# Optimization experiments

Measured on AMD Instinct MI355X. Metric: run time of the kernel, lower is better.

The kernel has to match this reference:

```python
import jax, jax.numpy as jnp
import numpy as np

NUM_HEADS = 16

def _apply_rope(t, cos, sin):
    # t: [B, nh, S, hd]; cos/sin: [S, hd//2]
    t1 = t[..., 0::2]
    t2 = t[..., 1::2]
    c = cos[None, None, :, :]
    s = sin[None, None, :, :]
    r1 = t1 * c - t2 * s
    r2 = t1 * s + t2 * c
    # interleave back to [..., hd]
    out = jnp.stack([r1, r2], axis=-1)
    return out.reshape(t.shape)

def setup_inputs() -> dict:
    key = jax.random.key(0)
    ks = jax.random.split(key, 6)
    B, S, H = 1, 4096, 1024
    hd = H // NUM_HEADS
    x = jax.random.normal(ks[0], (B, S, H), dtype=jnp.float32)
    # RoPE angle matrix: theta[pos, i] = pos / 10000^(2i/hd), shape [context, hd//2]
    pos = jnp.arange(S, dtype=jnp.float32)[:, None]
    inv_freq = 1.0 / (10000.0 ** (jnp.arange(0, hd, 2, dtype=jnp.float32) / hd))
    rotation = pos * inv_freq[None, :]
    sc = 1.0 / np.sqrt(H)
    W_qkv = jax.random.normal(ks[1], (H, 3 * H), dtype=jnp.float32) * sc
    b_qkv = jax.random.normal(ks[2], (3 * H,), dtype=jnp.float32) * 0.01
    W_out = jax.random.normal(ks[3], (H, H), dtype=jnp.float32) * sc
    b_out = jax.random.normal(ks[4], (H,), dtype=jnp.float32) * 0.01
    return {"x": x, "rotation": rotation, "W_qkv": W_qkv, "b_qkv": b_qkv,
            "W_out": W_out, "b_out": b_out, "window_size": 33}

def reference(x, rotation, W_qkv, b_qkv, W_out, b_out, window_size):
    B, S, H = x.shape
    nh = NUM_HEADS
    hd = H // nh
    W = window_size
    pad = W // 2
    qkv = x @ W_qkv + b_qkv                               # [B, S, 3H]
    qkv = qkv.reshape(B, S, nh, 3 * hd).transpose(0, 2, 1, 3)  # [B, nh, S, 3hd]
    q, k, v = jnp.split(qkv, 3, axis=-1)                  # each [B, nh, S, hd]
    cos = jnp.cos(rotation[:S])
    sin = jnp.sin(rotation[:S])
    q = _apply_rope(q, cos, sin)
    k = _apply_rope(k, cos, sin)
    # zero-pad along sequence, then gather sliding windows
    k_pad = jnp.pad(k, ((0, 0), (0, 0), (pad, pad), (0, 0)))
    v_pad = jnp.pad(v, ((0, 0), (0, 0), (pad, pad), (0, 0)))
    idx = jnp.arange(S)[:, None] + jnp.arange(W)[None, :]  # [S, W]
    k_win = k_pad[:, :, idx, :]                            # [B, nh, S, W, hd]
    v_win = v_pad[:, :, idx, :]
    scores = jnp.einsum('bnsh,bnswh->bnsw', q, k_win) / np.sqrt(hd)
    attn = jax.nn.softmax(scores, axis=-1)
    ctx = jnp.einsum('bnsw,bnswh->bnsh', attn, v_win)      # [B, nh, S, hd]
    ctx = ctx.transpose(0, 2, 1, 3).reshape(B, S, H)
    return ctx @ W_out + b_out
```

## Files before the change

kernel.cpp:

```cpp
#include <hip/hip_runtime.h>
#include <hip/hip_bf16.h>

#define S_LEN 4096
#define NH 16
#define HD 64
#define WIN 33
#define PAD 16
#define QT 64
#define KROWS 96
#define KPITCH_U 36

#define BM 128
#define BN 128
#define BK 64

typedef short short8 __attribute__((ext_vector_type(8)));
typedef float f32x4 __attribute__((ext_vector_type(4)));

__device__ __forceinline__ float bl(unsigned u){ return __uint_as_float(u << 16); }
__device__ __forceinline__ float bh(unsigned u){ return __uint_as_float(u & 0xffff0000u); }
__device__ __forceinline__ unsigned f2bfu(float f){
  unsigned u = __float_as_uint(f);
  return (u + 0x7fffu + ((u >> 16) & 1u)) >> 16;
}
__device__ __forceinline__ unsigned pack2(float a, float b){ return f2bfu(a) | (f2bfu(b) << 16); }

__device__ __forceinline__ void gload_lds16(const void* g, void* l){
  __builtin_amdgcn_global_load_lds(
      (const __attribute__((address_space(1))) void*)g,
      (__attribute__((address_space(3))) void*)l, 16, 0, 0);
}


__global__ __launch_bounds__(256) void rope_table(const float* __restrict__ rot,
                                                  float* __restrict__ cost,
                                                  float* __restrict__ sint, int n){
  int t = blockIdx.x * 256 + threadIdx.x;
  if (t < n) {
    float v = rot[t], sv, cv;
    sincosf(v, &sv, &cv);
    cost[t] = cv; sint[t] = sv;
  }
}

__global__ __launch_bounds__(256) void f32_to_bf16_vec(const float* __restrict__ in,
                                                       __hip_bfloat16* __restrict__ out){
  int t = blockIdx.x * 256 + threadIdx.x;
  const float4* p = (const float4*)in + (size_t)t * 2;
  float4 a = p[0], b = p[1];
  uint4 o;
  o.x = pack2(a.x, a.y); o.y = pack2(a.z, a.w);
  o.z = pack2(b.x, b.y); o.w = pack2(b.z, b.w);
  ((uint4*)out)[t] = o;
}

__global__ __launch_bounds__(256) void transpose_f32_to_bf16(const float* __restrict__ in,
                                                             __hip_bfloat16* __restrict__ out,
                                                             int R, int C){
  __shared__ float tile[32][33];
  int c0 = blockIdx.x * 32, r0 = blockIdx.y * 32;
  int tx = threadIdx.x, ty = threadIdx.y;
  #pragma unroll
  for (int i = 0; i < 4; ++i) {
    int r = ty + i * 8;
    tile[r][tx] = in[(size_t)(r0 + r) * C + c0 + tx];
  }
  __syncthreads();
  #pragma unroll
  for (int i = 0; i < 4; ++i) {
    int cc = ty + i * 8;
    ((unsigned short*)out)[(size_t)(c0 + cc) * R + r0 + tx] = (unsigned short)f2bfu(tile[tx][cc]);
  }
}


__global__ __launch_bounds__(256) void gemm_qkv_rope(
    const __hip_bfloat16* __restrict__ A,
    const __hip_bfloat16* __restrict__ Bt,
    const float* __restrict__ bias,
    const float* __restrict__ cost,
    const float* __restrict__ sint,
    unsigned short* __restrict__ Cout,
    int M, int N, int K)
{
  __shared__ unsigned int lA[BM * BK / 2];
  __shared__ unsigned int lB[BN * BK / 2];
  const int tid = threadIdx.x;
  const int wave = tid >> 6, lane = tid & 63;
  const int m0 = blockIdx.y * BM, n0 = blockIdx.x * BN;
  const int wm = (wave >> 1) * 64, wn = (wave & 1) * 64;
  const int l16 = lane >> 4, l15 = lane & 15;

  f32x4 acc[4][4];
  #pragma unroll
  for (int i = 0; i < 4; ++i)
    #pragma unroll
    for (int j = 0; j < 4; ++j) acc[i][j] = (f32x4){0.f, 0.f, 0.f, 0.f};

  const int nkt = K / BK;
  for (int kt = 0; kt < nkt; ++kt) {
    __syncthreads();
    #pragma unroll
    for (int it = 0; it < 4; ++it) {
      const int c = it * 256 + wave * 64 + lane;
      const int r = c >> 3, s8 = c & 7;
      const int ss = s8 ^ (r & 7);
      gload_lds16(A  + (size_t)(m0 + r) * K + kt * BK + ss * 8,
                  (char*)lA + (it * 256 + wave * 64) * 16);
      gload_lds16(Bt + (size_t)(n0 + r) * K + kt * BK + ss * 8,
                  (char*)lB + (it * 256 + wave * 64) * 16);
    }
    __syncthreads();
    #pragma unroll
    for (int ks = 0; ks < 2; ++ks) {
      short8 af[4], bfr[4];
      #pragma unroll
      for (int mi = 0; mi < 4; ++mi) {
        const int r = wm + mi * 16 + l15;
        const int slot = (ks * 4 + l16) ^ (r & 7);
        uint4 u = *(const uint4*)((const char*)lA + r * 128 + slot * 16);
        af[mi] = __builtin_bit_cast(short8, u);
      }
      #pragma unroll
      for (int ni = 0; ni < 4; ++ni) {
        const int r = wn + ni * 16 + l15;
        const int slot = (ks * 4 + l16) ^ (r & 7);
        uint4 u = *(const uint4*)((const char*)lB + r * 128 + slot * 16);
        bfr[ni] = __builtin_bit_cast(short8, u);
      }
      #pragma unroll
      for (int mi = 0; mi < 4; ++mi)
        #pragma unroll
        for (int ni = 0; ni < 4; ++ni)
          acc[mi][ni] = __builtin_amdgcn_mfma_f32_16x16x32_bf16(af[mi], bfr[ni], acc[mi][ni], 0, 0, 0);
    }
  }

  #pragma unroll
  for (int ni = 0; ni < 4; ++ni) {
    const int cn = n0 + wn + ni * 16 + l15;
    const int rseg = cn % 192;
    const float bv = bias[cn];
    if (rseg < 128) {
      const int i = (rseg & 63) >> 1;
      const float sgn = (cn & 1) ? 1.f : -1.f;
      #pragma unroll
      for (int mi = 0; mi < 4; ++mi) {
        #pragma unroll
        for (int j = 0; j < 4; ++j) {
          const int rm = m0 + wm + mi * 16 + l16 * 4 + j;
          const float v = acc[mi][ni][j] + bv;
          const float p = __shfl_xor(v, 1);
          const float cc = cost[rm * 32 + i], ss = sint[rm * 32 + i];
          const float res = v * cc + p * (sgn * ss);
          Cout[(size_t)rm * N + cn] = (unsigned short)f2bfu(res);
        }
      }
    } else {
      #pragma unroll
      for (int mi = 0; mi < 4; ++mi) {
        #pragma unroll
        for (int j = 0; j < 4; ++j) {
          const int rm = m0 + wm + mi * 16 + l16 * 4 + j;
          Cout[(size_t)rm * N + cn] = (unsigned short)f2bfu(acc[mi][ni][j] + bv);
        }
      }
    }
  }
}


__global__ __launch_bounds__(256) void gemm_small(
    const __hip_bfloat16* __restrict__ A,
    const __hip_bfloat16* __restrict__ Bt,
    const float* __restrict__ bias,
    float* __restrict__ Cout,
    int M, int N, int K)
{
  __shared__ unsigned int lA[64 * 64 / 2];
  __shared__ unsigned int lB[64 * 64 / 2];
  const int tid = threadIdx.x;
  const int wave = tid >> 6, lane = tid & 63;
  const int m0 = blockIdx.y * 64, n0 = blockIdx.x * 64;
  const int wm = (wave >> 1) * 32, wn = (wave & 1) * 32;
  const int l16 = lane >> 4, l15 = lane & 15;

  f32x4 acc[2][2];
  #pragma unroll
  for (int i = 0; i < 2; ++i)
    #pragma unroll
    for (int j = 0; j < 2; ++j) acc[i][j] = (f32x4){0.f, 0.f, 0.f, 0.f};

  const int nkt = K / 64;
  for (int kt = 0; kt < nkt; ++kt) {
    __syncthreads();
    #pragma unroll
    for (int it = 0; it < 2; ++it) {
      const int c = it * 256 + wave * 64 + lane;
      const int r = c >> 3, s8 = c & 7;
      const int ss = s8 ^ (r & 7);
      gload_lds16(A  + (size_t)(m0 + r) * K + kt * 64 + ss * 8,
                  (char*)lA + (it * 256 + wave * 64) * 16);
      gload_lds16(Bt + (size_t)(n0 + r) * K + kt * 64 + ss * 8,
                  (char*)lB + (it * 256 + wave * 64) * 16);
    }
    __syncthreads();
    #pragma unroll
    for (int ks = 0; ks < 2; ++ks) {
      short8 af[2], bfr[2];
      #pragma unroll
      for (int mi = 0; mi < 2; ++mi) {
        const int r = wm + mi * 16 + l15;
        const int slot = (ks * 4 + l16) ^ (r & 7);
        uint4 u = *(const uint4*)((const char*)lA + r * 128 + slot * 16);
        af[mi] = __builtin_bit_cast(short8, u);
      }
      #pragma unroll
      for (int ni = 0; ni < 2; ++ni) {
        const int r = wn + ni * 16 + l15;
        const int slot = (ks * 4 + l16) ^ (r & 7);
        uint4 u = *(const uint4*)((const char*)lB + r * 128 + slot * 16);
        bfr[ni] = __builtin_bit_cast(short8, u);
      }
      #pragma unroll
      for (int mi = 0; mi < 2; ++mi)
        #pragma unroll
        for (int ni = 0; ni < 2; ++ni)
          acc[mi][ni] = __builtin_amdgcn_mfma_f32_16x16x32_bf16(af[mi], bfr[ni], acc[mi][ni], 0, 0, 0);
    }
  }

  #pragma unroll
  for (int ni = 0; ni < 2; ++ni) {
    const int cn = n0 + wn + ni * 16 + l15;
    const float bv = bias[cn];
    #pragma unroll
    for (int mi = 0; mi < 2; ++mi) {
      #pragma unroll
      for (int j = 0; j < 4; ++j) {
        const int rm = m0 + wm + mi * 16 + l16 * 4 + j;
        Cout[(size_t)rm * N + cn] = acc[mi][ni][j] + bv;
      }
    }
  }
}


__global__ __launch_bounds__(256) void attn_kernel(const __hip_bfloat16* __restrict__ qkv,
                                                   __hip_bfloat16* __restrict__ ctx){
  __shared__ unsigned int kbuf[KROWS * KPITCH_U];
  __shared__ unsigned int vbuf[KROWS * KPITCH_U];
  const int tid = threadIdx.x;
  const int h   = blockIdx.x & 15;
  const int qs0 = (blockIdx.x >> 4) * QT;

  #pragma unroll
  for (int it = 0; it < 3; ++it) {
    int c = tid + it * 256;
    int r = c >> 3, s8 = c & 7;
    int srow = qs0 - PAD + r;
    uint4 kv = make_uint4(0, 0, 0, 0), vv = make_uint4(0, 0, 0, 0);
    if ((unsigned)srow < (unsigned)S_LEN) {
      kv = ((const uint4*)(qkv + (size_t)srow * 3072 + h * 192 + 64))[s8];
      vv = ((const uint4*)(qkv + (size_t)srow * 3072 + h * 192 + 128))[s8];
    }
    *(uint4*)(kbuf + r * KPITCH_U + s8 * 4) = kv;
    *(uint4*)(vbuf + r * KPITCH_U + s8 * 4) = vv;
  }

  const int ql = tid >> 2, t4 = tid & 3;
  const uint4* qp = (const uint4*)(qkv + (size_t)(qs0 + ql) * 3072 + h * 192);
  float qf[64];
  #pragma unroll
  for (int c = 0; c < 8; ++c) {
    uint4 v = qp[c];
    qf[c*8+0] = bl(v.x); qf[c*8+1] = bh(v.x);
    qf[c*8+2] = bl(v.y); qf[c*8+3] = bh(v.y);
    qf[c*8+4] = bl(v.z); qf[c*8+5] = bh(v.z);
    qf[c*8+6] = bl(v.w); qf[c*8+7] = bh(v.w);
  }
  __syncthreads();

  float sc[9];
  #pragma unroll
  for (int j = 0; j < 9; ++j) sc[j] = 0.f;
  float mx = -1e30f;
  #pragma unroll
  for (int j = 0; j < 9; ++j) {
    int w = t4 + 4 * j;
    if (w < WIN) {
      int rw = ql + w;
      const uint4* kp = (const uint4*)(kbuf + rw * KPITCH_U);
      float d = 0.f;
      #pragma unroll
      for (int c = 0; c < 8; ++c) {
        uint4 kv = kp[c];
        d += qf[c*8+0]*bl(kv.x) + qf[c*8+1]*bh(kv.x)
           + qf[c*8+2]*bl(kv.y) + qf[c*8+3]*bh(kv.y)
           + qf[c*8+4]*bl(kv.z) + qf[c*8+5]*bh(kv.z)
           + qf[c*8+6]*bl(kv.w) + qf[c*8+7]*bh(kv.w);
      }
      sc[j] = d * 0.125f;
      mx = fmaxf(mx, sc[j]);
    }
  }
  mx = fmaxf(mx, __shfl_xor(mx, 1));
  mx = fmaxf(mx, __shfl_xor(mx, 2));
  float sum = 0.f;
  #pragma unroll
  for (int j = 0; j < 9; ++j) {
    int w = t4 + 4 * j;
    if (w < WIN) { sc[j] = __expf(sc[j] - mx); sum += sc[j]; }
  }
  sum += __shfl_xor(sum, 1);
  sum += __shfl_xor(sum, 2);
  const float inv = 1.0f / sum;
  #pragma unroll
  for (int j = 0; j < 9; ++j) sc[j] *= inv;

  float accd[16];
  #pragma unroll
  for (int i = 0; i < 16; ++i) accd[i] = 0.f;
  #pragma unroll
  for (int w = 0; w < WIN; ++w) {
    float wgt = __shfl(sc[w >> 2], ((tid & 63) & ~3) | (w & 3), 64);
    int rw = ql + w;
    const uint4* vp = (const uint4*)(vbuf + rw * KPITCH_U + t4 * 8);
    uint4 a = vp[0], b = vp[1];
    float vf[16];
    vf[0]=bl(a.x); vf[1]=bh(a.x); vf[2]=bl(a.y); vf[3]=bh(a.y);
    vf[4]=bl(a.z); vf[5]=bh(a.z); vf[6]=bl(a.w); vf[7]=bh(a.w);
    vf[8]=bl(b.x); vf[9]=bh(b.x); vf[10]=bl(b.y); vf[11]=bh(b.y);
    vf[12]=bl(b.z); vf[13]=bh(b.z); vf[14]=bl(b.w); vf[15]=bh(b.w);
    #pragma unroll
    for (int i = 0; i < 16; ++i) accd[i] += wgt * vf[i];
  }

  unsigned short* op = (unsigned short*)ctx + (size_t)(qs0 + ql) * 1024 + h * 64 + t4 * 16;
  uint4 o1, o2;
  o1.x = pack2(accd[0], accd[1]);  o1.y = pack2(accd[2], accd[3]);
  o1.z = pack2(accd[4], accd[5]);  o1.w = pack2(accd[6], accd[7]);
  o2.x = pack2(accd[8], accd[9]);  o2.y = pack2(accd[10], accd[11]);
  o2.z = pack2(accd[12], accd[13]); o2.w = pack2(accd[14], accd[15]);
  *(uint4*)op = o1;
  *((uint4*)op + 1) = o2;
}


extern "C" void kernel_launch(void* const* d_in, const int* in_sizes, int n_in,
                              void* d_out, int out_size, void* d_ws, size_t ws_size,
                              hipStream_t stream)
{
  const float* x     = (const float*)d_in[0];
  const float* rot   = (const float*)d_in[1];
  const float* W_qkv = (const float*)d_in[2];
  const float* b_qkv = (const float*)d_in[3];
  const float* W_out = (const float*)d_in[4];
  const float* b_out = (const float*)d_in[5];
  float* out = (float*)d_out;

  char* ws = (char*)d_ws;
  __hip_bfloat16* xb   = (__hip_bfloat16*)(ws + 0);
  __hip_bfloat16* Wt1  = (__hip_bfloat16*)(ws + 8388608);
  __hip_bfloat16* Wt2  = (__hip_bfloat16*)(ws + 14680064);
  __hip_bfloat16* qkvb = (__hip_bfloat16*)(ws + 16777216);
  __hip_bfloat16* ctx  = (__hip_bfloat16*)(ws + 41943040);
  float* cost          = (float*)(ws + 50331648);
  float* sint          = (float*)(ws + 50855936);

  rope_table<<<512, 256, 0, stream>>>(rot, cost, sint, S_LEN * 32);
  f32_to_bf16_vec<<<2048, 256, 0, stream>>>(x, xb);
  transpose_f32_to_bf16<<<dim3(96, 32), dim3(32, 8), 0, stream>>>(W_qkv, Wt1, 1024, 3072);
  transpose_f32_to_bf16<<<dim3(32, 32), dim3(32, 8), 0, stream>>>(W_out, Wt2, 1024, 1024);
  gemm_qkv_rope<<<dim3(3072 / BN, 4096 / BM), 256, 0, stream>>>(xb, Wt1, b_qkv, cost, sint,
                                                                (unsigned short*)qkvb, 4096, 3072, 1024);
  attn_kernel<<<64 * 16, 256, 0, stream>>>(qkvb, ctx);
  gemm_small<<<dim3(1024 / 64, 4096 / 64), 256, 0, stream>>>(ctx, Wt2, b_out, out, 4096, 1024, 1024);
}
```

Measured before the change: 105.6 us.

## Merge prep kernels, double-buffer GEMMs, swizzle blocks, retile output GEMM

Merges the four preprocessing kernels (RoPE table, x conversion, two weight transposes) into one launch, and packs cos/sin into one float2 table computed with the fast __sincosf intrinsic. Both GEMMs now double-buffer LDS so the next K tile loads while the current one is multiplied. They also remap block indices for L2 locality and raise wave priority around the MFMA loops. The output GEMM moves from 64x64 to 128x64 tiles. The cost is more LDS per block, which may lower occupancy, and __sincosf gives less accurate sin/cos.

```diff
diff --git a/kernel.cpp b/kernel.cpp
--- a/kernel.cpp
+++ b/kernel.cpp
@@ -32,44 +32,44 @@
 }
 
 
-__global__ __launch_bounds__(256) void rope_table(const float* __restrict__ rot,
-                                                  float* __restrict__ cost,
-                                                  float* __restrict__ sint, int n){
-  int t = blockIdx.x * 256 + threadIdx.x;
-  if (t < n) {
+__global__ __launch_bounds__(256) void prep_all(
+    const float* __restrict__ rot, float2* __restrict__ csq,
+    const float* __restrict__ x, __hip_bfloat16* __restrict__ xb,
+    const float* __restrict__ Wq, __hip_bfloat16* __restrict__ Wt1,
+    const float* __restrict__ Wo, __hip_bfloat16* __restrict__ Wt2)
+{
+  __shared__ float tile[32][33];
+  const int b = blockIdx.x, tid = threadIdx.x;
+  if (b < 512) {
+    int t = b * 256 + tid;
     float v = rot[t], sv, cv;
-    sincosf(v, &sv, &cv);
-    cost[t] = cv; sint[t] = sv;
-  }
-}
-
-__global__ __launch_bounds__(256) void f32_to_bf16_vec(const float* __restrict__ in,
-                                                       __hip_bfloat16* __restrict__ out){
-  int t = blockIdx.x * 256 + threadIdx.x;
-  const float4* p = (const float4*)in + (size_t)t * 2;
-  float4 a = p[0], b = p[1];
-  uint4 o;
-  o.x = pack2(a.x, a.y); o.y = pack2(a.z, a.w);
-  o.z = pack2(b.x, b.y); o.w = pack2(b.z, b.w);
-  ((uint4*)out)[t] = o;
-}
-
-__global__ __launch_bounds__(256) void transpose_f32_to_bf16(const float* __restrict__ in,
-                                                             __hip_bfloat16* __restrict__ out,
-                                                             int R, int C){
-  __shared__ float tile[32][33];
-  int c0 = blockIdx.x * 32, r0 = blockIdx.y * 32;
-  int tx = threadIdx.x, ty = threadIdx.y;
-  #pragma unroll
-  for (int i = 0; i < 4; ++i) {
-    int r = ty + i * 8;
-    tile[r][tx] = in[(size_t)(r0 + r) * C + c0 + tx];
-  }
-  __syncthreads();
-  #pragma unroll
-  for (int i = 0; i < 4; ++i) {
-    int cc = ty + i * 8;
-    ((unsigned short*)out)[(size_t)(c0 + cc) * R + r0 + tx] = (unsigned short)f2bfu(tile[tx][cc]);
+    __sincosf(v, &sv, &cv);
+    csq[t] = make_float2(cv, sv);
+  } else if (b < 2560) {
+    int t = (b - 512) * 256 + tid;
+    const float4* p = (const float4*)x + (size_t)t * 2;
+    float4 a = p[0], c = p[1];
+    uint4 o;
+    o.x = pack2(a.x, a.y); o.y = pack2(a.z, a.w);
+    o.z = pack2(c.x, c.y); o.w = pack2(c.z, c.w);
+    ((uint4*)xb)[t] = o;
+  } else {
+    const float* in; unsigned short* out; int R, C, bx, by;
+    if (b < 5632) { int bb = b - 2560; in = Wq; out = (unsigned short*)Wt1; R = 1024; C = 3072; bx = bb % 96; by = bb / 96; }
+    else          { int bb = b - 5632; in = Wo; out = (unsigned short*)Wt2; R = 1024; C = 1024; bx = bb % 32; by = bb / 32; }
+    int c0 = bx * 32, r0 = by * 32;
+    int tx = tid & 31, ty = tid >> 5;
+    #pragma unroll
+    for (int i = 0; i < 4; ++i) {
+      int r = ty + i * 8;
+      tile[r][tx] = in[(size_t)(r0 + r) * C + c0 + tx];
+    }
+    __syncthreads();
+    #pragma unroll
+    for (int i = 0; i < 4; ++i) {
+      int cc = ty + i * 8;
+      out[(size_t)(c0 + cc) * R + r0 + tx] = (unsigned short)f2bfu(tile[tx][cc]);
+    }
   }
 }
 
@@ -78,16 +78,17 @@
     const __hip_bfloat16* __restrict__ A,
     const __hip_bfloat16* __restrict__ Bt,
     const float* __restrict__ bias,
-    const float* __restrict__ cost,
-    const float* __restrict__ sint,
+    const float2* __restrict__ csq,
     unsigned short* __restrict__ Cout,
     int M, int N, int K)
 {
-  __shared__ unsigned int lA[BM * BK / 2];
-  __shared__ unsigned int lB[BN * BK / 2];
+  __shared__ unsigned int lA[2][BM * BK / 2];
+  __shared__ unsigned int lB[2][BN * BK / 2];
   const int tid = threadIdx.x;
   const int wave = tid >> 6, lane = tid & 63;
-  const int m0 = blockIdx.y * BM, n0 = blockIdx.x * BN;
+  const int flat = blockIdx.y * 24 + blockIdx.x;
+  const int swz = (flat & 7) * 96 + (flat >> 3);
+  const int m0 = (swz / 24) * BM, n0 = (swz % 24) * BN;
   const int wm = (wave >> 1) * 64, wn = (wave & 1) * 64;
   const int l16 = lane >> 4, l15 = lane & 15;
 
@@ -97,20 +98,25 @@
     #pragma unroll
     for (int j = 0; j < 4; ++j) acc[i][j] = (f32x4){0.f, 0.f, 0.f, 0.f};
 
-  const int nkt = K / BK;
-  for (int kt = 0; kt < nkt; ++kt) {
-    __syncthreads();
+  auto stage = [&](int buf, int kt) {
     #pragma unroll
     for (int it = 0; it < 4; ++it) {
       const int c = it * 256 + wave * 64 + lane;
       const int r = c >> 3, s8 = c & 7;
       const int ss = s8 ^ (r & 7);
       gload_lds16(A  + (size_t)(m0 + r) * K + kt * BK + ss * 8,
-                  (char*)lA + (it * 256 + wave * 64) * 16);
+                  (char*)lA[buf] + (it * 256 + wave * 64) * 16);
       gload_lds16(Bt + (size_t)(n0 + r) * K + kt * BK + ss * 8,
-                  (char*)lB + (it * 256 + wave * 64) * 16);
-    }
-    __syncthreads();
+                  (char*)lB[buf] + (it * 256 + wave * 64) * 16);
+    }
+  };
+
+  const int nkt = K / BK;
+  stage(0, 0);
+  __syncthreads();
+  int cur = 0;
+  for (int kt = 0; kt < nkt; ++kt) {
+    if (kt + 1 < nkt) stage(cur ^ 1, kt + 1);
     #pragma unroll
     for (int ks = 0; ks < 2; ++ks) {
       short8 af[4], bfr[4];
@@ -118,22 +124,26 @@
       for (int mi = 0; mi < 4; ++mi) {
         const int r = wm + mi * 16 + l15;
         const int slot = (ks * 4 + l16) ^ (r & 7);
-        uint4 u = *(const uint4*)((const char*)lA + r * 128 + slot * 16);
+        uint4 u = *(const uint4*)((const char*)lA[cur] + r * 128 + slot * 16);
         af[mi] = __builtin_bit_cast(short8, u);
       }
       #pragma unroll
       for (int ni = 0; ni < 4; ++ni) {
         const int r = wn + ni * 16 + l15;
         const int slot = (ks * 4 + l16) ^ (r & 7);
-        uint4 u = *(const uint4*)((const char*)lB + r * 128 + slot * 16);
+        uint4 u = *(const uint4*)((const char*)lB[cur] + r * 128 + slot * 16);
         bfr[ni] = __builtin_bit_cast(short8, u);
       }
+      __builtin_amdgcn_s_setprio(1);
       #pragma unroll
       for (int mi = 0; mi < 4; ++mi)
         #pragma unroll
         for (int ni = 0; ni < 4; ++ni)
           acc[mi][ni] = __builtin_amdgcn_mfma_f32_16x16x32_bf16(af[mi], bfr[ni], acc[mi][ni], 0, 0, 0);
-    }
+      __builtin_amdgcn_s_setprio(0);
+    }
+    __syncthreads();
+    cur ^= 1;
   }
 
   #pragma unroll
@@ -151,9 +161,8 @@
           const int rm = m0 + wm + mi * 16 + l16 * 4 + j;
           const float v = acc[mi][ni][j] + bv;
           const float p = __shfl_xor(v, 1);
-          const float cc = cost[rm * 32 + i], ss = sint[rm * 32 + i];
-          const float res = v * cc + p * (sgn * ss);
-          Cout[(size_t)rm * N + cn] = (unsigned short)f2bfu(res);
+          const float2 cs = csq[rm * 32 + i];
+          Cout[(size_t)rm * N + cn] = (unsigned short)f2bfu(v * cs.x + p * (sgn * cs.y));
         }
       }
     } else {
@@ -170,64 +179,81 @@
 }
 
 
-__global__ __launch_bounds__(256) void gemm_small(
+__global__ __launch_bounds__(256) void gemm_out(
     const __hip_bfloat16* __restrict__ A,
     const __hip_bfloat16* __restrict__ Bt,
     const float* __restrict__ bias,
     float* __restrict__ Cout,
     int M, int N, int K)
 {
-  __shared__ unsigned int lA[64 * 64 / 2];
-  __shared__ unsigned int lB[64 * 64 / 2];
+  __shared__ unsigned int lA[2][128 * 64 / 2];
+  __shared__ unsigned int lB[2][64 * 64 / 2];
   const int tid = threadIdx.x;
   const int wave = tid >> 6, lane = tid & 63;
-  const int m0 = blockIdx.y * 64, n0 = blockIdx.x * 64;
-  const int wm = (wave >> 1) * 32, wn = (wave & 1) * 32;
+  const int flat = blockIdx.y * 16 + blockIdx.x;
+  const int swz = (flat & 7) * 64 + (flat >> 3);
+  const int m0 = (swz >> 4) * 128, n0 = (swz & 15) * 64;
+  const int wm = (wave >> 1) * 64, wn = (wave & 1) * 32;
   const int l16 = lane >> 4, l15 = lane & 15;
 
-  f32x4 acc[2][2];
-  #pragma unroll
-  for (int i = 0; i < 2; ++i)
+  f32x4 acc[4][2];
+  #pragma unroll
+  for (int i = 0; i < 4; ++i)
     #pragma unroll
     for (int j = 0; j < 2; ++j) acc[i][j] = (f32x4){0.f, 0.f, 0.f, 0.f};
 
-  const int nkt = K / 64;
-  for (int kt = 0; kt < nkt; ++kt) {
-    __syncthreads();
+  auto stage = [&](int buf, int kt) {
+    #pragma unroll
+    for (int it = 0; it < 4; ++it) {
+      const int c = it * 256 + wave * 64 + lane;
+      const int r = c >> 3, s8 = c & 7;
+      const int ss = s8 ^ (r & 7);
+      gload_lds16(A + (size_t)(m0 + r) * K + kt * 64 + ss * 8,
+                  (char*)lA[buf] + (it * 256 + wave * 64) * 16);
+    }
     #pragma unroll
     for (int it = 0; it < 2; ++it) {
       const int c = it * 256 + wave * 64 + lane;
       const int r = c >> 3, s8 = c & 7;
       const int ss = s8 ^ (r & 7);
-      gload_lds16(A  + (size_t)(m0 + r) * K + kt * 64 + ss * 8,
-                  (char*)lA + (it * 256 + wave * 64) * 16);
       gload_lds16(Bt + (size_t)(n0 + r) * K + kt * 64 + ss * 8,
-                  (char*)lB + (it * 256 + wave * 64) * 16);
-    }
-    __syncthreads();
+                  (char*)lB[buf] + (it * 256 + wave * 64) * 16);
+    }
+  };
+
+  const int nkt = K / 64;
+  stage(0, 0);
+  __syncthreads();
+  int cur = 0;
+  for (int kt = 0; kt < nkt; ++kt) {
+    if (kt + 1 < nkt) stage(cur ^ 1, kt + 1);
     #pragma unroll
     for (int ks = 0; ks < 2; ++ks) {
-      short8 af[2], bfr[2];
-      #pragma unroll
-      for (int mi = 0; mi < 2; ++mi) {
+      short8 af[4], bfr[2];
+      #pragma unroll
+      for (int mi = 0; mi < 4; ++mi) {
         const int r = wm + mi * 16 + l15;
         const int slot = (ks * 4 + l16) ^ (r & 7);
-        uint4 u = *(const uint4*)((const char*)lA + r * 128 + slot * 16);
+        uint4 u = *(const uint4*)((const char*)lA[cur] + r * 128 + slot * 16);
         af[mi] = __builtin_bit_cast(short8, u);
       }
       #pragma unroll
       for (int ni = 0; ni < 2; ++ni) {
         const int r = wn + ni * 16 + l15;
         const int slot = (ks * 4 + l16) ^ (r & 7);
-        uint4 u = *(const uint4*)((const char*)lB + r * 128 + slot * 16);
+        uint4 u = *(const uint4*)((const char*)lB[cur] + r * 128 + slot * 16);
         bfr[ni] = __builtin_bit_cast(short8, u);
       }
-      #pragma unroll
-      for (int mi = 0; mi < 2; ++mi)
+      __builtin_amdgcn_s_setprio(1);
+      #pragma unroll
+      for (int mi = 0; mi < 4; ++mi)
         #pragma unroll
         for (int ni = 0; ni < 2; ++ni)
           acc[mi][ni] = __builtin_amdgcn_mfma_f32_16x16x32_bf16(af[mi], bfr[ni], acc[mi][ni], 0, 0, 0);
-    }
+      __builtin_amdgcn_s_setprio(0);
+    }
+    __syncthreads();
+    cur ^= 1;
   }
 
   #pragma unroll
@@ -235,7 +261,7 @@
     const int cn = n0 + wn + ni * 16 + l15;
     const float bv = bias[cn];
     #pragma unroll
-    for (int mi = 0; mi < 2; ++mi) {
+    for (int mi = 0; mi < 4; ++mi) {
       #pragma unroll
       for (int j = 0; j < 4; ++j) {
         const int rm = m0 + wm + mi * 16 + l16 * 4 + j;
@@ -365,15 +391,11 @@
   __hip_bfloat16* Wt2  = (__hip_bfloat16*)(ws + 14680064);
   __hip_bfloat16* qkvb = (__hip_bfloat16*)(ws + 16777216);
   __hip_bfloat16* ctx  = (__hip_bfloat16*)(ws + 41943040);
-  float* cost          = (float*)(ws + 50331648);
-  float* sint          = (float*)(ws + 50855936);
-
-  rope_table<<<512, 256, 0, stream>>>(rot, cost, sint, S_LEN * 32);
-  f32_to_bf16_vec<<<2048, 256, 0, stream>>>(x, xb);
-  transpose_f32_to_bf16<<<dim3(96, 32), dim3(32, 8), 0, stream>>>(W_qkv, Wt1, 1024, 3072);
-  transpose_f32_to_bf16<<<dim3(32, 32), dim3(32, 8), 0, stream>>>(W_out, Wt2, 1024, 1024);
-  gemm_qkv_rope<<<dim3(3072 / BN, 4096 / BM), 256, 0, stream>>>(xb, Wt1, b_qkv, cost, sint,
+  float2* csq          = (float2*)(ws + 50331648);
+
+  prep_all<<<6656, 256, 0, stream>>>(rot, csq, x, xb, W_qkv, Wt1, W_out, Wt2);
+  gemm_qkv_rope<<<dim3(3072 / BN, 4096 / BM), 256, 0, stream>>>(xb, Wt1, b_qkv, csq,
                                                                 (unsigned short*)qkvb, 4096, 3072, 1024);
   attn_kernel<<<64 * 16, 256, 0, stream>>>(qkvb, ctx);
-  gemm_small<<<dim3(1024 / 64, 4096 / 64), 256, 0, stream>>>(ctx, Wt2, b_out, out, 4096, 1024, 1024);
-}
+  gemm_out<<<dim3(1024 / 64, 4096 / 128), 256, 0, stream>>>(ctx, Wt2, b_out, out, 4096, 1024, 1024);
+}
```

Result: faster. 95.23 us (-9.8%).
